# Optimization experiments

Hardware: AMD Instinct MI355X
Metric: run time of the kernel (lower is better)

The kernel has to match this reference:

```python
import jax, jax.numpy as jnp
import numpy as np

B, T, E, S, H = 1, 2048, 768, 256, 150
E3, E9 = 3 * E, 9 * E


def _lin(k, fan_in, fan_out):
    return jax.random.normal(k, (fan_in, fan_out), jnp.float32) / np.sqrt(fan_in).astype(np.float32)


def _mlp(x, W1, b1, W2, b2, W3, b3):
    # Score module: Linear -> ReLU -> Linear -> ReLU -> Linear (dropout = identity in eval)
    h = jax.nn.relu(x @ W1 + b1)
    h = jax.nn.relu(h @ W2 + b2)
    return h @ W3 + b3


def setup_inputs() -> dict:
    key = jax.random.key(0)
    ks = jax.random.split(key, 16)
    encoded_docs = jax.random.normal(ks[0], (B, T, E), jnp.float32)
    span_start = jnp.sort(jax.random.randint(ks[1], (B, S), 0, T - 16), axis=-1)
    span_width = jax.random.randint(ks[2], (B, S), 0, 16)
    return {
        'encoded_docs': encoded_docs,
        'span_start': span_start,
        'span_width': span_width,
        # attention Score (input dim E)
        'aW1': _lin(ks[3], E, H), 'ab1': jnp.zeros((H,), jnp.float32),
        'aW2': _lin(ks[4], H, H), 'ab2': jnp.zeros((H,), jnp.float32),
        'aW3': _lin(ks[5], H, 1), 'ab3': jnp.zeros((1,), jnp.float32),
        # mention Score (input dim 3E)
        'mW1': _lin(ks[6], E3, H), 'mb1': jnp.zeros((H,), jnp.float32),
        'mW2': _lin(ks[7], H, H), 'mb2': jnp.zeros((H,), jnp.float32),
        'mW3': _lin(ks[8], H, 1), 'mb3': jnp.zeros((1,), jnp.float32),
        # pairwise Score (input dim 9E)
        'pW1': _lin(ks[9], E9, H), 'pb1': jnp.zeros((H,), jnp.float32),
        'pW2': _lin(ks[10], H, H), 'pb2': jnp.zeros((H,), jnp.float32),
        'pW3': _lin(ks[11], H, 1), 'pb3': jnp.zeros((1,), jnp.float32),
    }


def reference(encoded_docs, span_start, span_width,
              aW1, ab1, aW2, ab2, aW3, ab3,
              mW1, mb1, mW2, mb2, mW3, mb3,
              pW1, pb1, pW2, pb2, pW3, pb3):
    e = encoded_docs  # [B, T, E]
    attn = _mlp(e, aW1, ab1, aW2, ab2, aW3, ab3)  # [B, T, 1]
    # span sums via prefix sums of attn-weighted embeddings (inclusive start..end)
    c = jnp.cumsum(e * attn, axis=1)  # [B, T, E]
    cpad = jnp.concatenate([jnp.zeros_like(c[:, :1]), c], axis=1)  # [B, T+1, E]
    end = jnp.clip(span_start + span_width, 0, T - 1)  # [B, S]
    bidx = jnp.arange(e.shape[0])[:, None]
    e_start = e[bidx, span_start]                      # [B, S, E]
    e_end = e[bidx, end]                               # [B, S, E]
    span_sum = cpad[bidx, end + 1] - cpad[bidx, span_start]  # [B, S, E]
    g = jnp.concatenate([e_start, e_end, span_sum], axis=-1)  # [B, S, 3E]
    m = _mlp(g, mW1, mb1, mW2, mb2, mW3, mb3)  # [B, S, 1]
    # pairwise: concat(g_i, g_j, g_i*g_j) @ pW1 decomposed over the three blocks
    Wa, Wb, Wc = pW1[:E3], pW1[E3:2 * E3], pW1[2 * E3:]
    hi = g @ Wa  # [B, S, H]
    hj = g @ Wb  # [B, S, H]
    hij = jnp.einsum('bie,bje,eh->bijh', g, g, Wc)  # [B, S, S, H]
    h1 = jax.nn.relu(hi[:, :, None, :] + hj[:, None, :, :] + hij + pb1)
    h2 = jax.nn.relu(h1 @ pW2 + pb2)
    s = h2 @ pW3 + pb3  # [B, S, S, 1]
    ext = (m[:, :, None, :] + m[:, None, :, :] + s) / 3.0
    return jnp.clip(ext, 0.0, 1.0)
```

## Files before the change

kernel.cpp:

```cpp
#include <hip/hip_runtime.h>

typedef unsigned short u16;
typedef unsigned int   u32;
typedef short bf16x8 __attribute__((ext_vector_type(8)));
typedef float f32x4  __attribute__((ext_vector_type(4)));

__device__ __forceinline__ u16 f2bf(float f) {
  union { float f; u32 u; } v; v.f = f;
  u32 u = v.u;
  u += 0x7fffu + ((u >> 16) & 1u);
  return (u16)(u >> 16);
}

__device__ __forceinline__ void splitbf(float x, u16& hi, u16& lo) {
  hi = f2bf(x);
  union { u32 u; float f; } r; r.u = (u32)hi << 16;
  lo = f2bf(x - r.f);
}

__device__ __forceinline__ float bflo(u32 p) {
  union { u32 u; float f; } v; v.u = p << 16; return v.f;
}
__device__ __forceinline__ float bfhi(u32 p) {
  union { u32 u; float f; } v; v.u = p & 0xffff0000u; return v.f;
}
__device__ __forceinline__ u32 cvtpk(float lo, float hi) {
  u32 r;
  asm("v_cvt_pk_bf16_f32 %0, %1, %2" : "=v"(r) : "v"(lo), "v"(hi));
  return r;
}
__device__ __forceinline__ void gload_lds16(const void* src, void* dst) {
  __builtin_amdgcn_global_load_lds(
      (const __attribute__((address_space(1))) u32*)src,
      (__attribute__((address_space(3))) u32*)dst, 16, 0, 0);
}

__global__ __launch_bounds__(256) void k_prepT(
    const float* __restrict__ mW1, const float* __restrict__ pW1,
    const float* __restrict__ aW1,
    u16* __restrict__ Wcath, u16* __restrict__ Wcatl,
    u16* __restrict__ aW1Th, u16* __restrict__ aW1Tl,
    u16* __restrict__ Wckg) {
  __shared__ float ls[64][153];
  const int tid = threadIdx.x;
  const int task = blockIdx.y;
  const int e0 = blockIdx.x * 64;
  if (task == 3 && e0 >= 768) return;
  const float* src;
  if (task == 0)      src = mW1;
  else if (task == 1) src = pW1;
  else if (task == 2) src = pW1 + (size_t)2304 * 150;
  else if (task == 3) src = aW1;
  else                src = pW1 + (size_t)4608 * 150;
  for (int t = tid; t < 9600; t += 256) {
    int r = t / 150, c = t - r * 150;
    ls[r][c] = src[(size_t)(e0 + r) * 150 + c];
  }
  __syncthreads();
  if (task < 3) {
    u16* dh = Wcath + (size_t)task * 160 * 2304;
    u16* dl = Wcatl + (size_t)task * 160 * 2304;
    for (int t = tid; t < 10240; t += 256) {
      int n = t >> 6, r = t & 63;
      float v = (n < 150) ? ls[r][n] : 0.f;
      u16 h, l; splitbf(v, h, l);
      dh[(size_t)n * 2304 + e0 + r] = h;
      dl[(size_t)n * 2304 + e0 + r] = l;
    }
  } else if (task == 3) {
    for (int t = tid; t < 10240; t += 256) {
      int n = t >> 6, r = t & 63;
      float v = (n < 150) ? ls[r][n] : 0.f;
      u16 h, l; splitbf(v, h, l);
      aW1Th[(size_t)n * 768 + e0 + r] = h;
      aW1Tl[(size_t)n * 768 + e0 + r] = l;
    }
  } else {
    for (int t = tid; t < 10240; t += 256) {
      int n = t >> 6, r = t & 63;
      int e = e0 + r;
      float v = (n < 150) ? ls[r][n] : 0.f;
      Wckg[((size_t)(e >> 3) * 160 + n) * 8 + (e & 7)] = f2bf(v);
    }
  }
}

__global__ __launch_bounds__(256) void k_prep0(
    const float* __restrict__ aW2, const float* __restrict__ mW2,
    const float* __restrict__ pW2, const float* __restrict__ pb1,
    const float* __restrict__ pb2, const float* __restrict__ pW3,
    float* __restrict__ aW2p, float* __restrict__ mW2p,
    u16* __restrict__ W2kg, float* __restrict__ pb1p,
    float* __restrict__ pb2p, float* __restrict__ w3p) {
  const int stride = gridDim.x * blockDim.x;
  const int t0 = blockIdx.x * blockDim.x + threadIdx.x;
  for (int t = t0; t < 152*160; t += stride) {
    int k = t / 160, h = t % 160;
    bool ok = (k < 150 && h < 150);
    aW2p[t] = ok ? aW2[k*150 + h] : 0.f;
    mW2p[t] = ok ? mW2[k*150 + h] : 0.f;
  }
  for (int t = t0; t < 24*1280; t += stride) {
    int kg = t / 1280, rem = t % 1280;
    int s = rem / 160, n = rem % 160;
    int k = kg*8 + s;
    float v = (k < 150 && n < 150) ? pW2[k*150 + n] : 0.f;
    W2kg[(size_t)kg*1280 + n*8 + s] = f2bf(v);
  }
  for (int t = t0; t < 160; t += stride) {
    pb1p[t] = (t < 150) ? pb1[t] : 0.f;
    pb2p[t] = (t < 150) ? pb2[t] : 0.f;
    w3p[t]  = (t < 150) ? pW3[t] : 0.f;
  }
}

__global__ __launch_bounds__(256) void k_attn1(
    const float* __restrict__ e, const u16* __restrict__ Wh,
    const u16* __restrict__ Wl, float* __restrict__ h1p) {
  __shared__ u16 lXh[32*64], lXl[32*64], lWh[160*64], lWl[160*64];
  const int tid = threadIdx.x, lane = tid & 63, w = tid >> 6;
  const int wm = w & 1, wh = w >> 1;
  const int m0 = blockIdx.x * 32;
  const int z  = blockIdx.y;
  f32x4 acc[5] = {};
  for (int e0 = z*384; e0 < (z+1)*384; e0 += 64) {
    {
      int r = tid >> 3, ec = tid & 7;
      const float* src = e + (size_t)(m0 + r)*768 + e0 + ec*8;
      float4 x0 = *(const float4*)src, x1 = *(const float4*)(src + 4);
      float xs[8] = {x0.x,x0.y,x0.z,x0.w,x1.x,x1.y,x1.z,x1.w};
      u16 hb[8], lb[8];
#pragma unroll
      for (int q = 0; q < 8; ++q) splitbf(xs[q], hb[q], lb[q]);
      int off = (r*128 + ec*16) ^ ((r & 7) << 4);
      *(uint4*)((char*)lXh + off) = make_uint4(
        (u32)hb[0]|((u32)hb[1]<<16), (u32)hb[2]|((u32)hb[3]<<16),
        (u32)hb[4]|((u32)hb[5]<<16), (u32)hb[6]|((u32)hb[7]<<16));
      *(uint4*)((char*)lXl + off) = make_uint4(
        (u32)lb[0]|((u32)lb[1]<<16), (u32)lb[2]|((u32)lb[3]<<16),
        (u32)lb[4]|((u32)lb[5]<<16), (u32)lb[6]|((u32)lb[7]<<16));
    }
#pragma unroll
    for (int t = 0; t < 5; ++t) {
      int c = tid + t*256;
      int h = c >> 3, ec = c & 7;
      int off = (h*128 + ec*16) ^ ((h & 7) << 4);
      *(uint4*)((char*)lWh + off) = *(const uint4*)(Wh + (size_t)h*768 + e0 + ec*8);
      *(uint4*)((char*)lWl + off) = *(const uint4*)(Wl + (size_t)h*768 + e0 + ec*8);
    }
    __syncthreads();
#pragma unroll
    for (int ks = 0; ks < 2; ++ks) {
      int eb = ks*64 + ((lane >> 4) << 4);
      int ar = wm*16 + (lane & 15);
      bf16x8 Ah = *(const bf16x8*)((const char*)lXh + ((ar*128 + eb) ^ ((ar & 7) << 4)));
      bf16x8 Al = *(const bf16x8*)((const char*)lXl + ((ar*128 + eb) ^ ((ar & 7) << 4)));
#pragma unroll
      for (int t = 0; t < 5; ++t) {
        int br = wh*80 + t*16 + (lane & 15);
        bf16x8 Bh = *(const bf16x8*)((const char*)lWh + ((br*128 + eb) ^ ((br & 7) << 4)));
        bf16x8 Bl = *(const bf16x8*)((const char*)lWl + ((br*128 + eb) ^ ((br & 7) << 4)));
        acc[t] = __builtin_amdgcn_mfma_f32_16x16x32_bf16(Ah, Bh, acc[t], 0, 0, 0);
        acc[t] = __builtin_amdgcn_mfma_f32_16x16x32_bf16(Al, Bh, acc[t], 0, 0, 0);
        acc[t] = __builtin_amdgcn_mfma_f32_16x16x32_bf16(Ah, Bl, acc[t], 0, 0, 0);
      }
    }
    __syncthreads();
  }
#pragma unroll
  for (int t = 0; t < 5; ++t) {
    int n = wh*80 + t*16 + (lane & 15);
#pragma unroll
    for (int r = 0; r < 4; ++r) {
      int m = m0 + wm*16 + ((lane >> 4) << 2) + r;
      h1p[((size_t)z*2048 + m)*160 + n] = acc[t][r];
    }
  }
}

__global__ __launch_bounds__(256) void k_attn2(
    const float* __restrict__ h1p, const float* __restrict__ W2p,
    const float* __restrict__ b1, const float* __restrict__ b2,
    const float* __restrict__ w3, const float* __restrict__ b3,
    float* __restrict__ attn) {
  __shared__ float hs[8][160];
  const int tid = threadIdx.x;
  const int t0 = blockIdx.x * 8;
  for (int idx = tid; idx < 1280; idx += 256) {
    int m = idx / 160, h = idx - m * 160;
    float s = h1p[(size_t)(t0 + m)*160 + h] + h1p[(size_t)(2048 + t0 + m)*160 + h];
    hs[m][h] = (h < 150) ? fmaxf(s + b1[h], 0.f) : 0.f;
  }
  __syncthreads();
  const int sp = tid >> 5, hb = tid & 31;
  float a2[5] = {0.f,0.f,0.f,0.f,0.f};
  for (int k = 0; k < 150; ++k) {
    float x = hs[sp][k];
#pragma unroll
    for (int q = 0; q < 5; ++q) a2[q] = fmaf(x, W2p[k*160 + hb + 32*q], a2[q]);
  }
  float p = 0.f;
#pragma unroll
  for (int q = 0; q < 5; ++q) {
    int h = hb + 32*q;
    if (h < 150) p += fmaxf(a2[q] + b2[h], 0.f) * w3[h];
  }
  p += __shfl_xor(p, 16, 32);
  p += __shfl_xor(p, 8, 32);
  p += __shfl_xor(p, 4, 32);
  p += __shfl_xor(p, 2, 32);
  p += __shfl_xor(p, 1, 32);
  if (hb == 0) attn[t0 + sp] = p + b3[0];
}

__global__ __launch_bounds__(256) void k_spans(
    const float* __restrict__ e, const float* __restrict__ attn,
    const int* __restrict__ sstart, const int* __restrict__ swidth,
    float* __restrict__ g, u16* __restrict__ gkg) {
  const int s = blockIdx.x;
  int st = sstart[s];
  int en = st + swidth[s];
  if (en > 2047) en = 2047;
  if (en < 0) en = 0;
  const int tid = threadIdx.x;
  for (int d = tid; d < 768; d += 256) {
    float v0 = e[(size_t)st*768 + d];
    float v1 = e[(size_t)en*768 + d];
    float acc = 0.f;
    for (int t = st; t <= en; ++t) acc += e[(size_t)t*768 + d] * attn[t];
    g[s*2304 + d]        = v0;
    g[s*2304 + 768 + d]  = v1;
    g[s*2304 + 1536 + d] = acc;
    int c0 = d, c1 = 768 + d, c2 = 1536 + d;
    gkg[((size_t)(c0>>3)*256 + s)*8 + (c0&7)] = f2bf(v0);
    gkg[((size_t)(c1>>3)*256 + s)*8 + (c1&7)] = f2bf(v1);
    gkg[((size_t)(c2>>3)*256 + s)*8 + (c2&7)] = f2bf(acc);
  }
}

__global__ __launch_bounds__(128) void k_span1(
    const float* __restrict__ g, const u16* __restrict__ Wh,
    const u16* __restrict__ Wl, float* __restrict__ pp) {
  __shared__ u16 lXh[16*64], lXl[16*64], lWh[160*64], lWl[160*64];
  const int tid = threadIdx.x, lane = tid & 63;
  const int wh = tid >> 6;
  const int m0 = blockIdx.x * 16;
  const int n0 = blockIdx.y * 160;
  const int z  = blockIdx.z;
  f32x4 acc[5] = {};
  for (int e0 = z*576; e0 < (z+1)*576; e0 += 64) {
    {
      int r = tid >> 3, ec = tid & 7;
      const float* src = g + (size_t)(m0 + r)*2304 + e0 + ec*8;
      float4 x0 = *(const float4*)src, x1 = *(const float4*)(src + 4);
      float xs[8] = {x0.x,x0.y,x0.z,x0.w,x1.x,x1.y,x1.z,x1.w};
      u16 hb[8], lb[8];
#pragma unroll
      for (int q = 0; q < 8; ++q) splitbf(xs[q], hb[q], lb[q]);
      int off = (r*128 + ec*16) ^ ((r & 7) << 4);
      *(uint4*)((char*)lXh + off) = make_uint4(
        (u32)hb[0]|((u32)hb[1]<<16), (u32)hb[2]|((u32)hb[3]<<16),
        (u32)hb[4]|((u32)hb[5]<<16), (u32)hb[6]|((u32)hb[7]<<16));
      *(uint4*)((char*)lXl + off) = make_uint4(
        (u32)lb[0]|((u32)lb[1]<<16), (u32)lb[2]|((u32)lb[3]<<16),
        (u32)lb[4]|((u32)lb[5]<<16), (u32)lb[6]|((u32)lb[7]<<16));
    }
#pragma unroll
    for (int t = 0; t < 10; ++t) {
      int c = tid + t*128;
      int h = c >> 3, ec = c & 7;
      int off = (h*128 + ec*16) ^ ((h & 7) << 4);
      *(uint4*)((char*)lWh + off) = *(const uint4*)(Wh + (size_t)(n0 + h)*2304 + e0 + ec*8);
      *(uint4*)((char*)lWl + off) = *(const uint4*)(Wl + (size_t)(n0 + h)*2304 + e0 + ec*8);
    }
    __syncthreads();
#pragma unroll
    for (int ks = 0; ks < 2; ++ks) {
      int eb = ks*64 + ((lane >> 4) << 4);
      int ar = lane & 15;
      bf16x8 Ah = *(const bf16x8*)((const char*)lXh + ((ar*128 + eb) ^ ((ar & 7) << 4)));
      bf16x8 Al = *(const bf16x8*)((const char*)lXl + ((ar*128 + eb) ^ ((ar & 7) << 4)));
#pragma unroll
      for (int t = 0; t < 5; ++t) {
        int br = wh*80 + t*16 + (lane & 15);
        bf16x8 Bh = *(const bf16x8*)((const char*)lWh + ((br*128 + eb) ^ ((br & 7) << 4)));
        bf16x8 Bl = *(const bf16x8*)((const char*)lWl + ((br*128 + eb) ^ ((br & 7) << 4)));
        acc[t] = __builtin_amdgcn_mfma_f32_16x16x32_bf16(Ah, Bh, acc[t], 0, 0, 0);
        acc[t] = __builtin_amdgcn_mfma_f32_16x16x32_bf16(Al, Bh, acc[t], 0, 0, 0);
        acc[t] = __builtin_amdgcn_mfma_f32_16x16x32_bf16(Ah, Bl, acc[t], 0, 0, 0);
      }
    }
    __syncthreads();
  }
#pragma unroll
  for (int t = 0; t < 5; ++t) {
    int nc = n0 + wh*80 + t*16 + (lane & 15);
#pragma unroll
    for (int r = 0; r < 4; ++r) {
      int m = m0 + ((lane >> 4) << 2) + r;
      pp[((size_t)z*256 + m)*480 + nc] = acc[t][r];
    }
  }
}

__global__ __launch_bounds__(256) void k_span1r(
    const float* __restrict__ pp, const float* __restrict__ mb1,
    float* __restrict__ mh1, float* __restrict__ hi, float* __restrict__ hj) {
  const int m = blockIdx.x;
  for (int n = threadIdx.x; n < 480; n += 256) {
    float s = 0.f;
#pragma unroll
    for (int z = 0; z < 4; ++z) s += pp[((size_t)z*256 + m)*480 + n];
    if (n < 160)      mh1[m*160 + n] = (n < 150) ? fmaxf(s + mb1[n], 0.f) : 0.f;
    else if (n < 320) hi[m*160 + n - 160] = s;
    else              hj[m*160 + n - 320] = s;
  }
}

__global__ __launch_bounds__(256) void k_span2(
    const float* __restrict__ mh1, const float* __restrict__ W2p,
    const float* __restrict__ b2, const float* __restrict__ w3,
    const float* __restrict__ b3, float* __restrict__ mo) {
  __shared__ float hs[8][160];
  const int tid = threadIdx.x;
  const int s0 = blockIdx.x * 8;
  for (int t = tid; t < 320; t += 256)
    ((float4*)&hs[0][0])[t] = ((const float4*)(mh1 + (size_t)s0*160))[t];
  __syncthreads();
  const int sp = tid >> 5, hb = tid & 31;
  float a2[5] = {0.f,0.f,0.f,0.f,0.f};
  for (int k = 0; k < 150; ++k) {
    float x = hs[sp][k];
#pragma unroll
    for (int q = 0; q < 5; ++q) a2[q] = fmaf(x, W2p[k*160 + hb + 32*q], a2[q]);
  }
  float p = 0.f;
#pragma unroll
  for (int q = 0; q < 5; ++q) {
    int h = hb + 32*q;
    if (h < 150) p += fmaxf(a2[q] + b2[h], 0.f) * w3[h];
  }
  p += __shfl_xor(p, 16, 32);
  p += __shfl_xor(p, 8, 32);
  p += __shfl_xor(p, 4, 32);
  p += __shfl_xor(p, 2, 32);
  p += __shfl_xor(p, 1, 32);
  if (hb == 0) mo[s0 + sp] = p + b3[0];
}

__global__ __launch_bounds__(512, 2) void k_hij5(
    const float* __restrict__ g, const u16* __restrict__ gkg,
    const u16* __restrict__ Wckg, const float* __restrict__ hi,
    const float* __restrict__ hj, const float* __restrict__ pb1p,
    const u16* __restrict__ W2kg, const float* __restrict__ pb2p,
    const float* __restrict__ w3p, const float* __restrict__ pb3,
    const float* __restrict__ mv, float* __restrict__ out) {
  __shared__ __align__(16) char smem[106496];
  const int tid = threadIdx.x, lane = tid & 63, w = tid >> 6;
  const int wj = w & 3, wh = w >> 2;
  const int i = blockIdx.x;
  const float* grow = g + (size_t)i * 2304;

  f32x4 acc[4][5] = {};
  uint4 wcR[3];
  float4 gA[3], gB[3];

  auto issueA = [&](int buf, int t) {
#pragma unroll
    for (int q = 0; q < 4; ++q) {
      const int base = (w * 4 + q) * 64;
      const int kg = base >> 8;
      const int jb = base & 255;
      const u16* src = gkg + (((size_t)(t * 8 + kg)) * 256 + jb + lane) * 8;
      gload_lds16(src, smem + buf * 32768 + base * 16);
    }
  };
  auto loadB = [&](int t) {
#pragma unroll
    for (int z = 0; z < 2; ++z) {
      int p = tid + z * 512;
      wcR[z] = *(const uint4*)(Wckg + ((size_t)t * 1280 + p) * 8);
      const float* gp = grow + t * 64 + (p / 160) * 8;
      gA[z] = *(const float4*)gp;
      gB[z] = *(const float4*)(gp + 4);
    }
    if (tid < 256) {
      int p = tid + 1024;
      wcR[2] = *(const uint4*)(Wckg + ((size_t)t * 1280 + p) * 8);
      const float* gp = grow + t * 64 + (p / 160) * 8;
      gA[2] = *(const float4*)gp;
      gB[2] = *(const float4*)(gp + 4);
    }
  };
  auto writeB = [&](int buf) {
    char* base = smem + 65536 + buf * 20480;
#pragma unroll
    for (int z = 0; z < 2; ++z) {
      int p = tid + z * 512;
      uint4 v = wcR[z]; float4 ga = gA[z], gb = gB[z];
      uint4 r;
      r.x = cvtpk(bflo(v.x) * ga.x, bfhi(v.x) * ga.y);
      r.y = cvtpk(bflo(v.y) * ga.z, bfhi(v.y) * ga.w);
      r.z = cvtpk(bflo(v.z) * gb.x, bfhi(v.z) * gb.y);
      r.w = cvtpk(bflo(v.w) * gb.z, bfhi(v.w) * gb.w);
      *(uint4*)(base + p * 16) = r;
    }
    if (tid < 256) {
      int p = tid + 1024;
      uint4 v = wcR[2]; float4 ga = gA[2], gb = gB[2];
      uint4 r;
      r.x = cvtpk(bflo(v.x) * ga.x, bfhi(v.x) * ga.y);
      r.y = cvtpk(bflo(v.y) * ga.z, bfhi(v.y) * ga.w);
      r.z = cvtpk(bflo(v.z) * gb.x, bfhi(v.z) * gb.y);
      r.w = cvtpk(bflo(v.w) * gb.z, bfhi(v.w) * gb.w);
      *(uint4*)(base + p * 16) = r;
    }
  };

  issueA(0, 0);
  loadB(0);
  writeB(0);
  __syncthreads();

  for (int t = 0; t < 36; ++t) {
    const int buf = t & 1;
    if (t < 35) { issueA(buf ^ 1, t + 1); loadB(t + 1); }
    const char* Ab = smem + buf * 32768;
    const char* Bb = smem + 65536 + buf * 20480;
    __builtin_amdgcn_s_setprio(1);
#pragma unroll
    for (int ks = 0; ks < 2; ++ks) {
      const int kgl = ks * 4 + (lane >> 4);
      bf16x8 af[4];
#pragma unroll
      for (int q = 0; q < 4; ++q)
        af[q] = *(const bf16x8*)(Ab + (kgl * 256 + wj * 64 + q * 16 + (lane & 15)) * 16);
#pragma unroll
      for (int u = 0; u < 5; ++u) {
        bf16x8 bfr = *(const bf16x8*)(Bb + (kgl * 160 + wh * 80 + u * 16 + (lane & 15)) * 16);
#pragma unroll
        for (int q = 0; q < 4; ++q)
          acc[q][u] = __builtin_amdgcn_mfma_f32_16x16x32_bf16(af[q], bfr, acc[q][u], 0, 0, 0);
      }
    }
    __builtin_amdgcn_s_setprio(0);
    if (t < 35) writeB(buf ^ 1);
    __syncthreads();
  }

  {
    float hib[5];
#pragma unroll
    for (int u = 0; u < 5; ++u) {
      int h = wh * 80 + u * 16 + (lane & 15);
      hib[u] = hi[i * 160 + h] + pb1p[h];
    }
#pragma unroll
    for (int q = 0; q < 4; ++q) {
      int jl = wj * 64 + q * 16 + ((lane >> 4) << 2);
#pragma unroll
      for (int r = 0; r < 4; ++r) {
        const float* hjr = hj + (size_t)(jl + r) * 160;
#pragma unroll
        for (int u = 0; u < 5; ++u) {
          int h = wh * 80 + u * 16 + (lane & 15);
          float v = fmaxf(acc[q][u][r] + hib[u] + hjr[h], 0.f);
          *(u16*)(smem + ((h >> 3) * 256 + jl + r) * 16 + (h & 7) * 2) = f2bf(v);
        }
      }
    }
  }
  __syncthreads();

  f32x4 acc2[4][5] = {};
  for (int c = 0; c < 3; ++c) {
    const int G64 = (c < 2) ? 20 : 10;
    for (int g0 = w; g0 < G64; g0 += 8) {
      const u16* src = W2kg + ((size_t)c * 1280 + g0 * 64 + lane) * 8;
      gload_lds16(src, smem + 81920 + g0 * 1024);
    }
    __syncthreads();
    const int nks = (c < 2) ? 2 : 1;
    for (int ks = 0; ks < nks; ++ks) {
      const int kl = ks * 4 + (lane >> 4);
      bf16x8 af2[4];
#pragma unroll
      for (int q = 0; q < 4; ++q)
        af2[q] = *(const bf16x8*)(smem + ((c * 8 + kl) * 256 + wj * 64 + q * 16 + (lane & 15)) * 16);
#pragma unroll
      for (int u = 0; u < 5; ++u) {
        bf16x8 b2 = *(const bf16x8*)(smem + 81920 + (kl * 160 + wh * 80 + u * 16 + (lane & 15)) * 16);
#pragma unroll
        for (int q = 0; q < 4; ++q)
          acc2[q][u] = __builtin_amdgcn_mfma_f32_16x16x32_bf16(af2[q], b2, acc2[q][u], 0, 0, 0);
      }
    }
    __syncthreads();
  }

  {
    float w3v[5], b2v[5];
#pragma unroll
    for (int u = 0; u < 5; ++u) {
      int h2 = wh * 80 + u * 16 + (lane & 15);
      w3v[u] = w3p[h2]; b2v[u] = pb2p[h2];
    }
#pragma unroll
    for (int q = 0; q < 4; ++q) {
#pragma unroll
      for (int r = 0; r < 4; ++r) {
        float sp = 0.f;
#pragma unroll
        for (int u = 0; u < 5; ++u)
          sp += fmaxf(acc2[q][u][r] + b2v[u], 0.f) * w3v[u];
        sp += __shfl_xor(sp, 1);
        sp += __shfl_xor(sp, 2);
        sp += __shfl_xor(sp, 4);
        sp += __shfl_xor(sp, 8);
        if ((lane & 15) == 0) {
          int jl = wj * 64 + q * 16 + ((lane >> 4) << 2) + r;
          *(float*)(smem + 102400 + (jl * 2 + wh) * 4) = sp;
        }
      }
    }
  }
  __syncthreads();
  if (tid < 256) {
    float s = *(const float*)(smem + 102400 + tid * 8) +
              *(const float*)(smem + 102400 + tid * 8 + 4) + pb3[0];
    float v = (mv[i] + mv[tid] + s) * (1.f / 3.f);
    out[i * 256 + tid] = fminf(fmaxf(v, 0.f), 1.f);
  }
}

extern "C" void kernel_launch(void* const* d_in, const int* in_sizes, int n_in,
                              void* d_out, int out_size, void* d_ws, size_t ws_size,
                              hipStream_t stream) {
  (void)in_sizes; (void)n_in; (void)out_size; (void)ws_size;
  const float* e    = (const float*)d_in[0];
  const int*   sst  = (const int*)d_in[1];
  const int*   swd  = (const int*)d_in[2];
  const float* aW1  = (const float*)d_in[3];
  const float* ab1  = (const float*)d_in[4];
  const float* aW2  = (const float*)d_in[5];
  const float* ab2  = (const float*)d_in[6];
  const float* aW3  = (const float*)d_in[7];
  const float* ab3  = (const float*)d_in[8];
  const float* mW1  = (const float*)d_in[9];
  const float* mb1  = (const float*)d_in[10];
  const float* mW2  = (const float*)d_in[11];
  const float* mb2  = (const float*)d_in[12];
  const float* mW3  = (const float*)d_in[13];
  const float* mb3  = (const float*)d_in[14];
  const float* pW1  = (const float*)d_in[15];
  const float* pb1  = (const float*)d_in[16];
  const float* pW2  = (const float*)d_in[17];
  const float* pb2  = (const float*)d_in[18];
  const float* pW3  = (const float*)d_in[19];
  const float* pb3  = (const float*)d_in[20];
  float* out = (float*)d_out;

  char* ws = (char*)d_ws;
  size_t off = 0;
  auto alloc = [&](size_t bytes) -> char* {
    char* p = ws + off;
    off += (bytes + 255) & ~(size_t)255;
    return p;
  };
  float* attn  = (float*)alloc(2048ULL*4);
  float* g     = (float*)alloc(256ULL*2304*4);
  float* hi    = (float*)alloc(256ULL*160*4);
  float* hj    = (float*)alloc(256ULL*160*4);
  float* mv    = (float*)alloc(256ULL*4);
  float* h1p   = (float*)alloc(2ULL*2048*160*4);
  float* mh1   = (float*)alloc(256ULL*160*4);
  float* pp    = (float*)alloc(4ULL*256*480*4);
  u16*   aW1Th = (u16*)alloc(160ULL*768*2);
  u16*   aW1Tl = (u16*)alloc(160ULL*768*2);
  u16*   Wcath = (u16*)alloc(480ULL*2304*2);
  u16*   Wcatl = (u16*)alloc(480ULL*2304*2);
  float* aW2p  = (float*)alloc(152ULL*160*4);
  float* mW2p  = (float*)alloc(152ULL*160*4);
  u16*   gkg   = (u16*)alloc(288ULL*256*8*2);
  u16*   Wckg  = (u16*)alloc(288ULL*160*8*2);
  u16*   W2kg  = (u16*)alloc(24ULL*1280*2);
  float* pb1p  = (float*)alloc(160ULL*4);
  float* pb2p  = (float*)alloc(160ULL*4);
  float* w3p   = (float*)alloc(160ULL*4);

  k_prepT<<<dim3(36, 5), 256, 0, stream>>>(mW1, pW1, aW1,
                                           Wcath, Wcatl, aW1Th, aW1Tl, Wckg);
  k_prep0<<<128, 256, 0, stream>>>(aW2, mW2, pW2, pb1, pb2, pW3,
                                   aW2p, mW2p, W2kg, pb1p, pb2p, w3p);
  k_attn1<<<dim3(64, 2), 256, 0, stream>>>(e, aW1Th, aW1Tl, h1p);
  k_attn2<<<256, 256, 0, stream>>>(h1p, aW2p, ab1, ab2, aW3, ab3, attn);
  k_spans<<<256, 256, 0, stream>>>(e, attn, sst, swd, g, gkg);
  k_span1<<<dim3(16, 3, 4), 128, 0, stream>>>(g, Wcath, Wcatl, pp);
  k_span1r<<<256, 256, 0, stream>>>(pp, mb1, mh1, hi, hj);
  k_span2<<<32, 256, 0, stream>>>(mh1, mW2p, mb2, mW3, mb3, mv);
  k_hij5<<<256, 512, 0, stream>>>(g, gkg, Wckg, hi, hj, pb1p,
                                  W2kg, pb2p, w3p, pb3, mv, out);
}
```

Before: 141.1 us.

## Load hij A-operand straight to registers and merge small prep and reduce kernels

The pairwise hij kernel now loads the g-tile A fragments from global memory directly into registers, prefetching the next step's fragments after the MFMA loop. It drops the LDS double buffer for A, so only B is staged in LDS. The small weight-prep kernel is folded into k_prepT as an extra grid row, and the split-K reduction is fused into the mention-MLP second layer, removing two launches and the mh1 buffer. The trade-off is higher register pressure from eight bf16x8 fragments held per thread, and exposed global-load latency on the A path.

After: 138.3 us. No clear change (-2.0%).

```diff
diff --git a/kernel.cpp b/kernel.cpp
--- a/kernel.cpp
+++ b/kernel.cpp
@@ -37,14 +37,43 @@
 
 __global__ __launch_bounds__(256) void k_prepT(
     const float* __restrict__ mW1, const float* __restrict__ pW1,
-    const float* __restrict__ aW1,
+    const float* __restrict__ aW1, const float* __restrict__ aW2,
+    const float* __restrict__ mW2, const float* __restrict__ pW2,
+    const float* __restrict__ pb1, const float* __restrict__ pb2,
+    const float* __restrict__ pW3,
     u16* __restrict__ Wcath, u16* __restrict__ Wcatl,
     u16* __restrict__ aW1Th, u16* __restrict__ aW1Tl,
-    u16* __restrict__ Wckg) {
+    u16* __restrict__ Wckg,
+    float* __restrict__ aW2p, float* __restrict__ mW2p,
+    u16* __restrict__ W2kg, float* __restrict__ pb1p,
+    float* __restrict__ pb2p, float* __restrict__ w3p) {
   __shared__ float ls[64][153];
   const int tid = threadIdx.x;
   const int task = blockIdx.y;
   const int e0 = blockIdx.x * 64;
+  if (task == 5) {
+    const int stride = 36 * 256;
+    const int t0 = blockIdx.x * 256 + tid;
+    for (int t = t0; t < 152*160; t += stride) {
+      int k = t / 160, h = t % 160;
+      bool ok = (k < 150 && h < 150);
+      aW2p[t] = ok ? aW2[k*150 + h] : 0.f;
+      mW2p[t] = ok ? mW2[k*150 + h] : 0.f;
+    }
+    for (int t = t0; t < 24*1280; t += stride) {
+      int kg = t / 1280, rem = t % 1280;
+      int s = rem / 160, n = rem % 160;
+      int k = kg*8 + s;
+      float v = (k < 150 && n < 150) ? pW2[k*150 + n] : 0.f;
+      W2kg[(size_t)kg*1280 + n*8 + s] = f2bf(v);
+    }
+    for (int t = t0; t < 160; t += stride) {
+      pb1p[t] = (t < 150) ? pb1[t] : 0.f;
+      pb2p[t] = (t < 150) ? pb2[t] : 0.f;
+      w3p[t]  = (t < 150) ? pW3[t] : 0.f;
+    }
+    return;
+  }
   if (task == 3 && e0 >= 768) return;
   const float* src;
   if (task == 0)      src = mW1;
@@ -82,35 +111,6 @@
       float v = (n < 150) ? ls[r][n] : 0.f;
       Wckg[((size_t)(e >> 3) * 160 + n) * 8 + (e & 7)] = f2bf(v);
     }
-  }
-}
-
-__global__ __launch_bounds__(256) void k_prep0(
-    const float* __restrict__ aW2, const float* __restrict__ mW2,
-    const float* __restrict__ pW2, const float* __restrict__ pb1,
-    const float* __restrict__ pb2, const float* __restrict__ pW3,
-    float* __restrict__ aW2p, float* __restrict__ mW2p,
-    u16* __restrict__ W2kg, float* __restrict__ pb1p,
-    float* __restrict__ pb2p, float* __restrict__ w3p) {
-  const int stride = gridDim.x * blockDim.x;
-  const int t0 = blockIdx.x * blockDim.x + threadIdx.x;
-  for (int t = t0; t < 152*160; t += stride) {
-    int k = t / 160, h = t % 160;
-    bool ok = (k < 150 && h < 150);
-    aW2p[t] = ok ? aW2[k*150 + h] : 0.f;
-    mW2p[t] = ok ? mW2[k*150 + h] : 0.f;
-  }
-  for (int t = t0; t < 24*1280; t += stride) {
-    int kg = t / 1280, rem = t % 1280;
-    int s = rem / 160, n = rem % 160;
-    int k = kg*8 + s;
-    float v = (k < 150 && n < 150) ? pW2[k*150 + n] : 0.f;
-    W2kg[(size_t)kg*1280 + n*8 + s] = f2bf(v);
-  }
-  for (int t = t0; t < 160; t += stride) {
-    pb1p[t] = (t < 150) ? pb1[t] : 0.f;
-    pb2p[t] = (t < 150) ? pb2[t] : 0.f;
-    w3p[t]  = (t < 150) ? pW3[t] : 0.f;
   }
 }
 
@@ -303,29 +303,24 @@
   }
 }
 
-__global__ __launch_bounds__(256) void k_span1r(
+__global__ __launch_bounds__(256) void k_span2r(
     const float* __restrict__ pp, const float* __restrict__ mb1,
-    float* __restrict__ mh1, float* __restrict__ hi, float* __restrict__ hj) {
-  const int m = blockIdx.x;
-  for (int n = threadIdx.x; n < 480; n += 256) {
-    float s = 0.f;
-#pragma unroll
-    for (int z = 0; z < 4; ++z) s += pp[((size_t)z*256 + m)*480 + n];
-    if (n < 160)      mh1[m*160 + n] = (n < 150) ? fmaxf(s + mb1[n], 0.f) : 0.f;
-    else if (n < 320) hi[m*160 + n - 160] = s;
-    else              hj[m*160 + n - 320] = s;
-  }
-}
-
-__global__ __launch_bounds__(256) void k_span2(
-    const float* __restrict__ mh1, const float* __restrict__ W2p,
-    const float* __restrict__ b2, const float* __restrict__ w3,
-    const float* __restrict__ b3, float* __restrict__ mo) {
+    const float* __restrict__ W2p, const float* __restrict__ b2,
+    const float* __restrict__ w3, const float* __restrict__ b3,
+    float* __restrict__ hi, float* __restrict__ hj, float* __restrict__ mo) {
   __shared__ float hs[8][160];
   const int tid = threadIdx.x;
   const int s0 = blockIdx.x * 8;
-  for (int t = tid; t < 320; t += 256)
-    ((float4*)&hs[0][0])[t] = ((const float4*)(mh1 + (size_t)s0*160))[t];
+  for (int idx = tid; idx < 3840; idx += 256) {
+    int mr = idx / 480, n = idx - mr * 480;
+    int m = s0 + mr;
+    float s = 0.f;
+#pragma unroll
+    for (int z = 0; z < 4; ++z) s += pp[((size_t)z*256 + m)*480 + n];
+    if (n < 160)      hs[mr][n] = (n < 150) ? fmaxf(s + mb1[n], 0.f) : 0.f;
+    else if (n < 320) hi[m*160 + n - 160] = s;
+    else              hj[m*160 + n - 320] = s;
+  }
   __syncthreads();
   const int sp = tid >> 5, hb = tid & 31;
   float a2[5] = {0.f,0.f,0.f,0.f,0.f};
@@ -348,103 +343,96 @@
   if (hb == 0) mo[s0 + sp] = p + b3[0];
 }
 
-__global__ __launch_bounds__(512, 2) void k_hij5(
+__global__ __launch_bounds__(512, 2) void k_hij6(
     const float* __restrict__ g, const u16* __restrict__ gkg,
     const u16* __restrict__ Wckg, const float* __restrict__ hi,
     const float* __restrict__ hj, const float* __restrict__ pb1p,
     const u16* __restrict__ W2kg, const float* __restrict__ pb2p,
     const float* __restrict__ w3p, const float* __restrict__ pb3,
     const float* __restrict__ mv, float* __restrict__ out) {
-  __shared__ __align__(16) char smem[106496];
+  __shared__ __align__(16) char smem[104448];
   const int tid = threadIdx.x, lane = tid & 63, w = tid >> 6;
   const int wj = w & 3, wh = w >> 2;
   const int i = blockIdx.x;
   const float* grow = g + (size_t)i * 2304;
 
   f32x4 acc[4][5] = {};
+  bf16x8 afC[8];
   uint4 wcR[3];
   float4 gA[3], gB[3];
 
-  auto issueA = [&](int buf, int t) {
-#pragma unroll
-    for (int q = 0; q < 4; ++q) {
-      const int base = (w * 4 + q) * 64;
-      const int kg = base >> 8;
-      const int jb = base & 255;
-      const u16* src = gkg + (((size_t)(t * 8 + kg)) * 256 + jb + lane) * 8;
-      gload_lds16(src, smem + buf * 32768 + base * 16);
-    }
+  const u16* pA = gkg + (((lane >> 4) * 256) + wj * 64 + (lane & 15)) * 8;
+  const int ep0 = (tid / 160) * 8;
+  const int ep1 = ((tid + 512) / 160) * 8;
+  const int ep2 = ((tid + 1024) / 160) * 8;
+  const int bB = (((lane >> 4) * 160) + wh * 80 + (lane & 15)) * 16;
+
+  auto loadA = [&](int t) {
+    const u16* p = pA + (size_t)t * 16384;
+#pragma unroll
+    for (int ks = 0; ks < 2; ++ks)
+#pragma unroll
+      for (int q = 0; q < 4; ++q)
+        afC[ks * 4 + q] = *(const bf16x8*)(p + ks * 8192 + q * 128);
   };
   auto loadB = [&](int t) {
-#pragma unroll
-    for (int z = 0; z < 2; ++z) {
-      int p = tid + z * 512;
-      wcR[z] = *(const uint4*)(Wckg + ((size_t)t * 1280 + p) * 8);
-      const float* gp = grow + t * 64 + (p / 160) * 8;
-      gA[z] = *(const float4*)gp;
-      gB[z] = *(const float4*)(gp + 4);
-    }
+    const u16* wp = Wckg + (size_t)t * 10240;
+    const float* gp = grow + t * 64;
+    wcR[0] = *(const uint4*)(wp + (size_t)tid * 8);
+    gA[0] = *(const float4*)(gp + ep0); gB[0] = *(const float4*)(gp + ep0 + 4);
+    wcR[1] = *(const uint4*)(wp + (size_t)(tid + 512) * 8);
+    gA[1] = *(const float4*)(gp + ep1); gB[1] = *(const float4*)(gp + ep1 + 4);
     if (tid < 256) {
-      int p = tid + 1024;
-      wcR[2] = *(const uint4*)(Wckg + ((size_t)t * 1280 + p) * 8);
-      const float* gp = grow + t * 64 + (p / 160) * 8;
-      gA[2] = *(const float4*)gp;
-      gB[2] = *(const float4*)(gp + 4);
+      wcR[2] = *(const uint4*)(wp + (size_t)(tid + 1024) * 8);
+      gA[2] = *(const float4*)(gp + ep2); gB[2] = *(const float4*)(gp + ep2 + 4);
     }
   };
   auto writeB = [&](int buf) {
-    char* base = smem + 65536 + buf * 20480;
+    char* base = smem + buf * 20480;
 #pragma unroll
     for (int z = 0; z < 2; ++z) {
-      int p = tid + z * 512;
       uint4 v = wcR[z]; float4 ga = gA[z], gb = gB[z];
       uint4 r;
       r.x = cvtpk(bflo(v.x) * ga.x, bfhi(v.x) * ga.y);
       r.y = cvtpk(bflo(v.y) * ga.z, bfhi(v.y) * ga.w);
       r.z = cvtpk(bflo(v.z) * gb.x, bfhi(v.z) * gb.y);
       r.w = cvtpk(bflo(v.w) * gb.z, bfhi(v.w) * gb.w);
-      *(uint4*)(base + p * 16) = r;
+      *(uint4*)(base + (tid + z * 512) * 16) = r;
     }
     if (tid < 256) {
-      int p = tid + 1024;
       uint4 v = wcR[2]; float4 ga = gA[2], gb = gB[2];
       uint4 r;
       r.x = cvtpk(bflo(v.x) * ga.x, bfhi(v.x) * ga.y);
       r.y = cvtpk(bflo(v.y) * ga.z, bfhi(v.y) * ga.w);
       r.z = cvtpk(bflo(v.z) * gb.x, bfhi(v.z) * gb.y);
       r.w = cvtpk(bflo(v.w) * gb.z, bfhi(v.w) * gb.w);
-      *(uint4*)(base + p * 16) = r;
+      *(uint4*)(base + (tid + 1024) * 16) = r;
     }
   };
 
-  issueA(0, 0);
+  loadA(0);
   loadB(0);
   writeB(0);
   __syncthreads();
 
   for (int t = 0; t < 36; ++t) {
     const int buf = t & 1;
-    if (t < 35) { issueA(buf ^ 1, t + 1); loadB(t + 1); }
-    const char* Ab = smem + buf * 32768;
-    const char* Bb = smem + 65536 + buf * 20480;
+    if (t < 35) loadB(t + 1);
+    const char* Bb = smem + buf * 20480;
     __builtin_amdgcn_s_setprio(1);
 #pragma unroll
     for (int ks = 0; ks < 2; ++ks) {
-      const int kgl = ks * 4 + (lane >> 4);
-      bf16x8 af[4];
-#pragma unroll
-      for (int q = 0; q < 4; ++q)
-        af[q] = *(const bf16x8*)(Ab + (kgl * 256 + wj * 64 + q * 16 + (lane & 15)) * 16);
 #pragma unroll
       for (int u = 0; u < 5; ++u) {
-        bf16x8 bfr = *(const bf16x8*)(Bb + (kgl * 160 + wh * 80 + u * 16 + (lane & 15)) * 16);
+        bf16x8 bfr = *(const bf16x8*)(Bb + bB + ks * 10240 + u * 256);
 #pragma unroll
         for (int q = 0; q < 4; ++q)
-          acc[q][u] = __builtin_amdgcn_mfma_f32_16x16x32_bf16(af[q], bfr, acc[q][u], 0, 0, 0);
+          acc[q][u] = __builtin_amdgcn_mfma_f32_16x16x32_bf16(
+              afC[ks * 4 + q], bfr, acc[q][u], 0, 0, 0);
       }
     }
     __builtin_amdgcn_s_setprio(0);
-    if (t < 35) writeB(buf ^ 1);
+    if (t < 35) { loadA(t + 1); writeB(buf ^ 1); }
     __syncthreads();
   }
 
@@ -573,7 +561,6 @@
   float* hj    = (float*)alloc(256ULL*160*4);
   float* mv    = (float*)alloc(256ULL*4);
   float* h1p   = (float*)alloc(2ULL*2048*160*4);
-  float* mh1   = (float*)alloc(256ULL*160*4);
   float* pp    = (float*)alloc(4ULL*256*480*4);
   u16*   aW1Th = (u16*)alloc(160ULL*768*2);
   u16*   aW1Tl = (u16*)alloc(160ULL*768*2);
@@ -588,16 +575,15 @@
   float* pb2p  = (float*)alloc(160ULL*4);
   float* w3p   = (float*)alloc(160ULL*4);
 
-  k_prepT<<<dim3(36, 5), 256, 0, stream>>>(mW1, pW1, aW1,
-                                           Wcath, Wcatl, aW1Th, aW1Tl, Wckg);
-  k_prep0<<<128, 256, 0, stream>>>(aW2, mW2, pW2, pb1, pb2, pW3,
-                                   aW2p, mW2p, W2kg, pb1p, pb2p, w3p);
+  k_prepT<<<dim3(36, 6), 256, 0, stream>>>(mW1, pW1, aW1, aW2, mW2, pW2,
+                                           pb1, pb2, pW3,
+                                           Wcath, Wcatl, aW1Th, aW1Tl, Wckg,
+                                           aW2p, mW2p, W2kg, pb1p, pb2p, w3p);
   k_attn1<<<dim3(64, 2), 256, 0, stream>>>(e, aW1Th, aW1Tl, h1p);
   k_attn2<<<256, 256, 0, stream>>>(h1p, aW2p, ab1, ab2, aW3, ab3, attn);
   k_spans<<<256, 256, 0, stream>>>(e, attn, sst, swd, g, gkg);
   k_span1<<<dim3(16, 3, 4), 128, 0, stream>>>(g, Wcath, Wcatl, pp);
-  k_span1r<<<256, 256, 0, stream>>>(pp, mb1, mh1, hi, hj);
-  k_span2<<<32, 256, 0, stream>>>(mh1, mW2p, mb2, mW3, mb3, mv);
-  k_hij5<<<256, 512, 0, stream>>>(g, gkg, Wckg, hi, hj, pb1p,
+  k_span2r<<<32, 256, 0, stream>>>(pp, mb1, mW2p, mb2, mW3, mb3, hi, hj, mv);
+  k_hij6<<<256, 512, 0, stream>>>(g, gkg, Wckg, hi, hj, pb1p,
                                   W2kg, pb2p, w3p, pb3, mv, out);
 }
```
